# Kernel tuning notes

Hardware: AMD Instinct MI355X
Metric: run time of the kernel (lower is better)

## Reference

```python
import jax, jax.numpy as jnp
import numpy as np

MODEL_DIM = 2048
NUM_HEADS = 16
NUM_KV_HEADS = 4
HEAD_DIM = MODEL_DIM // NUM_HEADS  # 128
ROPE_BASE = 10000.0
LOCAL_WINDOW = 1024
EPS = 1.1920929e-07  # torch.finfo(float32).eps, F.rms_norm default
NEG = -1e30


def setup_inputs() -> dict:
    key = jax.random.key(0)
    ks = jax.random.split(key, 5)
    s = 0.02
    return {
        "x": jax.random.normal(ks[0], (1, 4096, MODEL_DIM), jnp.float32),
        "Wq": jax.random.normal(ks[1], (MODEL_DIM, MODEL_DIM), jnp.float32) * s,
        "Wk": jax.random.normal(ks[2], (NUM_KV_HEADS * HEAD_DIM, MODEL_DIM), jnp.float32) * s,
        "Wv": jax.random.normal(ks[3], (NUM_KV_HEADS * HEAD_DIM, MODEL_DIM), jnp.float32) * s,
        "Wo": jax.random.normal(ks[4], (MODEL_DIM, MODEL_DIM), jnp.float32) * s,
    }


def _rms_norm(x):
    return x * jax.lax.rsqrt(jnp.mean(x * x, axis=-1, keepdims=True) + EPS)


def _rope_tables(seqlen, dtype):
    inv_freq = 1.0 / (ROPE_BASE ** (jnp.arange(0, HEAD_DIM, 2, dtype=jnp.float32) / HEAD_DIM))
    freqs = jnp.arange(seqlen, dtype=jnp.float32)[:, None] * inv_freq[None, :]  # [S, hd/2]
    return jnp.cos(freqs).astype(dtype), jnp.sin(freqs).astype(dtype)


def _apply_rope(x, cos, sin):
    # x: [B, H, S, hd]; cos/sin: [S, hd/2]
    half = x.shape[-1] // 2
    x1, x2 = x[..., :half], x[..., half:]
    c = cos[None, None, :, :]
    s = sin[None, None, :, :]
    return jnp.concatenate((x1 * c + x2 * s, x2 * c - x1 * s), axis=-1)


def reference(x, Wq, Wk, Wv, Wo):
    B, S, _ = x.shape
    G = NUM_HEADS // NUM_KV_HEADS
    q = (x @ Wq.T).reshape(B, S, NUM_HEADS, HEAD_DIM).transpose(0, 2, 1, 3)
    k = (x @ Wk.T).reshape(B, S, NUM_KV_HEADS, HEAD_DIM).transpose(0, 2, 1, 3)
    v = (x @ Wv.T).reshape(B, S, NUM_KV_HEADS, HEAD_DIM).transpose(0, 2, 1, 3)
    q = _rms_norm(q)
    k = _rms_norm(k)
    cos, sin = _rope_tables(S, q.dtype)
    q = _apply_rope(q, cos, sin)
    k = _apply_rope(k, cos, sin)
    # GQA: expand kv heads to match query heads
    k = jnp.repeat(k, G, axis=1)  # [B, H, S, hd]
    v = jnp.repeat(v, G, axis=1)
    scale = 1.0 / np.sqrt(HEAD_DIM)
    scores = jnp.einsum("bhqd,bhkd->bhqk", q, k) * scale  # [B, H, S, S]
    idx = jnp.arange(S)
    causal = idx[None, :] <= idx[:, None]
    in_window = idx[None, :] > idx[:, None] - LOCAL_WINDOW
    allowed = causal & in_window  # [S, S]
    scores = jnp.where(allowed[None, None, :, :], scores, NEG)
    probs = jax.nn.softmax(scores, axis=-1)
    y = jnp.einsum("bhqk,bhkd->bhqd", probs, v)  # [B, H, S, hd]
    y = y.transpose(0, 2, 1, 3).reshape(B, S, MODEL_DIM)
    return y @ Wo.T
```

## Files before the change

kernel.cpp:

```cpp
#include <hip/hip_runtime.h>

typedef short bf16x8 __attribute__((ext_vector_type(8)));
typedef short short4v __attribute__((ext_vector_type(4)));
typedef float f32x4 __attribute__((ext_vector_type(4)));

__device__ __forceinline__ ushort f2b(float f) {
  union { float f; unsigned u; } v; v.f = f;
  unsigned r = v.u + 0x7FFF + ((v.u >> 16) & 1);
  return (ushort)(r >> 16);
}
__device__ __forceinline__ float b2f(ushort u) {
  union { unsigned u; float f; } v; v.u = ((unsigned)u) << 16;
  return v.f;
}
__device__ __forceinline__ unsigned cvtpk(float lo, float hi) {
  unsigned r;
  asm volatile("v_cvt_pk_bf16_f32 %0, %1, %2" : "=v"(r) : "v"(lo), "v"(hi));
  return r;
}
__device__ __forceinline__ f32x4 mfma16(bf16x8 a, bf16x8 b, f32x4 c) {
  return __builtin_amdgcn_mfma_f32_16x16x32_bf16(a, b, c, 0, 0, 0);
}

#define GLD_LDS16(g, l) \
  __builtin_amdgcn_global_load_lds((const __attribute__((address_space(1))) void*)(g), \
                                   (__attribute__((address_space(3))) void*)(l), 16, 0, 0)

__global__ __launch_bounds__(256) void cast_bf16(const float* __restrict__ in,
                                                 ushort* __restrict__ out, int n4) {
  int i = blockIdx.x * 256 + threadIdx.x;
  if (i >= n4) return;
  float4 f = ((const float4*)in)[i];
  ushort4 u;
  u.x = f2b(f.x); u.y = f2b(f.y); u.z = f2b(f.z); u.w = f2b(f.w);
  ((ushort4*)out)[i] = u;
}

__global__ void rope_tables_k(float* __restrict__ cosT, float* __restrict__ sinT) {
  int s = blockIdx.x, i = threadIdx.x;
  float inv = powf(10000.0f, -(float)i * (1.0f / 64.0f));
  float f = (float)s * inv;
  cosT[s * 64 + i] = cosf(f);
  sinT[s * 64 + i] = sinf(f);
}

template <bool BF16OUT>
__global__ __launch_bounds__(512) void gemm256(const ushort* __restrict__ A,
                                               const ushort* __restrict__ B,
                                               void* __restrict__ Cout,
                                               int M, int N, int K) {
  __shared__ __align__(16) ushort lds[65536];
  const int t = threadIdx.x;
  const int lane = t & 63, w = t >> 6;
  const int wr = w & 3, wc = w >> 2;
  const int l15 = lane & 15, l4 = lane >> 4;
  const int nbn = N >> 7;
  const long m0 = (long)(blockIdx.x / nbn) * 256;
  const long n0 = (long)(blockIdx.x % nbn) * 128;
  const int nk = K >> 6;

  const int rd0 = l15 * 32 + l4 * 8;
  const int rdoff = rd0 ^ ((((rd0 >> 6) & 3)) << 3);

  int arow[4], acol[4], brow[2], bcol[2];
#pragma unroll
  for (int r = 0; r < 4; ++r) {
    int us = r * 4096 + t * 8;
    int uu = us ^ (((us >> 6) & 3) << 3);
    int sub = uu >> 9;
    arow[r] = (sub >> 1) * 16 + ((uu >> 5) & 15);
    acol[r] = (sub & 1) * 32 + (uu & 31);
    if (r < 2) { brow[r] = arow[r]; bcol[r] = acol[r]; }
  }

#define STAGE_A(kk, slot)                                                      \
  do {                                                                         \
    _Pragma("unroll") for (int r = 0; r < 4; ++r)                              \
        GLD_LDS16(A + (m0 + arow[r]) * K + (kk) + acol[r],                     \
                  &lds[(slot) * 16384 + r * 4096 + t * 8]);                    \
  } while (0)
#define STAGE_B(kk, slot)                                                      \
  do {                                                                         \
    _Pragma("unroll") for (int r = 0; r < 2; ++r)                              \
        GLD_LDS16(B + (n0 + brow[r]) * K + (kk) + bcol[r],                     \
                  &lds[49152 + (slot) * 8192 + r * 4096 + t * 8]);             \
  } while (0)

  f32x4 acc[4][4] = {};

  STAGE_A(0, 0);
  STAGE_B(0, 0);
  STAGE_A(64, 1);

  for (int j = 0; j < nk; ++j) {
    const int sa = j % 3, sb = j & 1;
    asm volatile("s_waitcnt vmcnt(4)" ::: "memory");
    __builtin_amdgcn_s_barrier();

    {
      int kn = j + 1; if (kn > nk - 1) kn = nk - 1;
      STAGE_B(kn * 64, (j + 1) & 1);
    }
    bf16x8 bfrag[4][2], afrag[2][2];
#pragma unroll
    for (int n = 0; n < 4; ++n)
#pragma unroll
      for (int ks = 0; ks < 2; ++ks)
        bfrag[n][ks] = *(const bf16x8*)(&lds[49152 + sb * 8192 +
                                             ((wc * 4 + n) * 2 + ks) * 512 + rdoff]);
#pragma unroll
    for (int i = 0; i < 2; ++i)
#pragma unroll
      for (int ks = 0; ks < 2; ++ks)
        afrag[i][ks] = *(const bf16x8*)(&lds[sa * 16384 +
                                             ((wr * 4 + i) * 2 + ks) * 512 + rdoff]);
    __builtin_amdgcn_s_setprio(1);
#pragma unroll
    for (int i = 0; i < 2; ++i)
#pragma unroll
      for (int n = 0; n < 4; ++n)
#pragma unroll
        for (int ks = 0; ks < 2; ++ks)
          acc[i][n] = mfma16(afrag[i][ks], bfrag[n][ks], acc[i][n]);
    __builtin_amdgcn_s_setprio(0);
    __builtin_amdgcn_s_barrier();

    {
      int kn = j + 2; if (kn > nk - 1) kn = nk - 1;
      STAGE_A(kn * 64, (j + 2) % 3);
    }
    bf16x8 afrag1[2][2];
#pragma unroll
    for (int i = 0; i < 2; ++i)
#pragma unroll
      for (int ks = 0; ks < 2; ++ks)
        afrag1[i][ks] = *(const bf16x8*)(&lds[sa * 16384 +
                                              ((wr * 4 + i + 2) * 2 + ks) * 512 + rdoff]);
    __builtin_amdgcn_s_setprio(1);
#pragma unroll
    for (int i = 0; i < 2; ++i)
#pragma unroll
      for (int n = 0; n < 4; ++n)
#pragma unroll
        for (int ks = 0; ks < 2; ++ks)
          acc[i + 2][n] = mfma16(afrag1[i][ks], bfrag[n][ks], acc[i + 2][n]);
    __builtin_amdgcn_s_setprio(0);
  }
  asm volatile("s_waitcnt vmcnt(0)" ::: "memory");

#pragma unroll
  for (int i = 0; i < 4; ++i) {
#pragma unroll
    for (int n = 0; n < 4; ++n) {
      long mrow = m0 + wr * 64 + i * 16 + l4 * 4;
      long ncol = n0 + wc * 64 + n * 16 + l15;
#pragma unroll
      for (int r = 0; r < 4; ++r) {
        if constexpr (BF16OUT)
          ((ushort*)Cout)[(mrow + r) * N + ncol] = f2b(acc[i][n][r]);
        else
          ((float*)Cout)[(mrow + r) * N + ncol] = acc[i][n][r];
      }
    }
  }
#undef STAGE_A
#undef STAGE_B
}

__global__ __launch_bounds__(256) void postproc_k(const ushort* __restrict__ qkvb,
                                                  const float* __restrict__ cosT,
                                                  const float* __restrict__ sinT,
                                                  ushort* __restrict__ qb,
                                                  ushort* __restrict__ kb,
                                                  ushort* __restrict__ vtb) {
  const int lane = threadIdx.x & 63;
  const int s = blockIdx.x * 4 + (threadIdx.x >> 6);
  const int h = blockIdx.y;
  const int colbase = (h < 16) ? h * 128 : (h < 20 ? 2048 + (h - 16) * 128
                                                   : 2560 + (h - 20) * 128);
  const ushort* row = qkvb + (long)s * 3072 + colbase;
  float x1 = b2f(row[lane]), x2 = b2f(row[lane + 64]);
  if (h >= 20) {
    int kvh = h - 20;
    vtb[(long)(kvh * 128 + lane) * 4096 + s]      = f2b(x1);
    vtb[(long)(kvh * 128 + lane + 64) * 4096 + s] = f2b(x2);
    return;
  }
  float ss = x1 * x1 + x2 * x2;
#pragma unroll
  for (int m = 1; m < 64; m <<= 1) ss += __shfl_xor(ss, m);
  float rn = rsqrtf(ss * (1.0f / 128.0f) + 1.1920929e-07f);
  float c = cosT[s * 64 + lane], sn = sinT[s * 64 + lane];
  float x1n = x1 * rn, x2n = x2 * rn;
  float o1 = x1n * c + x2n * sn;
  float o2 = x2n * c - x1n * sn;
  if (h < 16) {
    const float scq = 0.08838834764831845f;
    ushort* dst = qb + ((long)h * 4096 + s) * 128;
    dst[lane] = f2b(o1 * scq);
    dst[lane + 64] = f2b(o2 * scq);
  } else {
    ushort* dst = kb + ((long)(h - 16) * 4096 + s) * 128;
    dst[lane] = f2b(o1);
    dst[lane + 64] = f2b(o2);
  }
}

__global__ __launch_bounds__(512) void attn_k(const ushort* __restrict__ qb,
                                              const ushort* __restrict__ kb,
                                              const ushort* __restrict__ vtb,
                                              ushort* __restrict__ yb) {
  __shared__ __align__(16) ushort lds[32768];
  const int t = threadIdx.x;
  const int lane = t & 63, w = t >> 6;
  const int l15 = lane & 15, l4 = lane >> 4;
  const int q0 = ((int)gridDim.x - 1 - (int)blockIdx.x) * 128;
  const int h = blockIdx.y, kvh = h >> 2;
  const int qw = q0 + w * 16;
  const int q = qw + l15;
  const int swz = l15 & 7;

  const ushort* Qp = qb + ((long)h * 4096 + q) * 128 + l4 * 8;
  bf16x8 qf[4];
#pragma unroll
  for (int c = 0; c < 4; ++c) qf[c] = *(const bf16x8*)(Qp + c * 32);

  const ushort* Kg = kb + (long)kvh * 4096 * 128;
  const ushort* Vg = vtb + (long)kvh * 128 * 4096;

  int kb_lo = q0 - 1023; if (kb_lo < 0) kb_lo = 0; kb_lo &= ~63;
  const int nt = (q0 + 127 - kb_lo) / 64 + 1;

  const int lbuA = (0 * 8 + w) * 512 + lane * 8;
  const int lbuB = (1 * 8 + w) * 512 + lane * 8;
  const int krA = lbuA >> 7, kcA = ((lbuA >> 3) & 15) ^ (krA & 7);
  const int krB = lbuB >> 7, kcB = ((lbuB >> 3) & 15) ^ (krB & 7);
  const int vrA = lbuA >> 6, vcA = ((lbuA >> 3) & 7) ^ (vrA & 7);
  const int vrB = lbuB >> 6, vcB = ((lbuB >> 3) & 7) ^ (vrB & 7);

#define STAGE(kbs, b)                                                        \
  do {                                                                       \
    ushort* Kl_ = &lds[(b) * 16384];                                         \
    ushort* Vl_ = &lds[(b) * 16384 + 8192];                                  \
    GLD_LDS16(Kg + (long)((kbs) + krA) * 128 + kcA * 8, Kl_ + lbuA);         \
    GLD_LDS16(Kg + (long)((kbs) + krB) * 128 + kcB * 8, Kl_ + lbuB);         \
    GLD_LDS16(Vg + (long)vrA * 4096 + (kbs) + vcA * 8, Vl_ + lbuA);          \
    GLD_LDS16(Vg + (long)vrB * 4096 + (kbs) + vcB * 8, Vl_ + lbuB);          \
  } while (0)

  f32x4 o[8] = {};
  float mrun = -1e30f, lrun = 0.0f;

  STAGE(kb_lo, 0);
  asm volatile("s_waitcnt vmcnt(0)" ::: "memory");
  __syncthreads();

  for (int ti = 0; ti < nt; ++ti) {
    const int kbs = kb_lo + ti * 64;
    const int cur = ti & 1;
    if (ti + 1 < nt) STAGE(kbs + 64, cur ^ 1);

    if (kbs + 63 >= qw - 1023 && kbs <= qw + 15) {
      const ushort* Kl = &lds[cur * 16384];
      const ushort* Vl = &lds[cur * 16384 + 8192];

      f32x4 sc[4];
#pragma unroll
      for (int st = 0; st < 4; ++st) {
        sc[st] = f32x4{0.f, 0.f, 0.f, 0.f};
        const ushort* kr = Kl + (st * 16 + l15) * 128;
#pragma unroll
        for (int c = 0; c < 4; ++c)
          sc[st] = mfma16(*(const bf16x8*)(kr + (((c * 4 + l4) ^ swz) * 8)), qf[c], sc[st]);
      }

      float s[16];
#pragma unroll
      for (int st = 0; st < 4; ++st)
#pragma unroll
        for (int r = 0; r < 4; ++r) {
          const int ki = kbs + st * 16 + l4 * 4 + r;
          s[st * 4 + r] = (ki <= q && ki > q - 1024) ? sc[st][r] : -1e30f;
        }

      float m0a = fmaxf(fmaxf(s[0], s[1]), fmaxf(s[2], s[3]));
      float m1a = fmaxf(fmaxf(s[4], s[5]), fmaxf(s[6], s[7]));
      float m2a = fmaxf(fmaxf(s[8], s[9]), fmaxf(s[10], s[11]));
      float m3a = fmaxf(fmaxf(s[12], s[13]), fmaxf(s[14], s[15]));
      float mx = fmaxf(fmaxf(m0a, m1a), fmaxf(m2a, m3a));
      mx = fmaxf(mx, __shfl_xor(mx, 16));
      mx = fmaxf(mx, __shfl_xor(mx, 32));

      float mn;
      if (__all(mx <= mrun + 8.0f)) {
        mn = mrun;
      } else {
        mn = fmaxf(mrun, mx);
        const float corr = __expf(mrun - mn);
        mrun = mn;
#pragma unroll
        for (int db = 0; db < 8; ++db)
#pragma unroll
          for (int r = 0; r < 4; ++r) o[db][r] *= corr;
        lrun *= corr;
      }

      float p[16];
#pragma unroll
      for (int j = 0; j < 16; ++j) p[j] = __expf(s[j] - mn);
      float ps = ((p[0] + p[1]) + (p[2] + p[3])) + ((p[4] + p[5]) + (p[6] + p[7]));
      ps += ((p[8] + p[9]) + (p[10] + p[11])) + ((p[12] + p[13]) + (p[14] + p[15]));
      ps += __shfl_xor(ps, 16);
      ps += __shfl_xor(ps, 32);
      lrun += ps;

      union { unsigned u[4]; bf16x8 v; } pa, pb;
      pa.u[0] = cvtpk(p[0], p[1]);   pa.u[1] = cvtpk(p[2], p[3]);
      pa.u[2] = cvtpk(p[4], p[5]);   pa.u[3] = cvtpk(p[6], p[7]);
      pb.u[0] = cvtpk(p[8], p[9]);   pb.u[1] = cvtpk(p[10], p[11]);
      pb.u[2] = cvtpk(p[12], p[13]); pb.u[3] = cvtpk(p[14], p[15]);

      const int co = 4 * (l4 & 1);
      const int c0 = (l4 >> 1) ^ swz, c1 = (2 + (l4 >> 1)) ^ swz;
      const int c2 = (4 + (l4 >> 1)) ^ swz, c3 = (6 + (l4 >> 1)) ^ swz;
#pragma unroll
      for (int db = 0; db < 8; ++db) {
        const ushort* vr = Vl + (db * 16 + l15) * 64;
        short4v a0 = *(const short4v*)(vr + c0 * 8 + co);
        short4v a1 = *(const short4v*)(vr + c1 * 8 + co);
        bf16x8 va = __builtin_shufflevector(a0, a1, 0, 1, 2, 3, 4, 5, 6, 7);
        o[db] = mfma16(va, pa.v, o[db]);
        short4v b0 = *(const short4v*)(vr + c2 * 8 + co);
        short4v b1 = *(const short4v*)(vr + c3 * 8 + co);
        bf16x8 vb = __builtin_shufflevector(b0, b1, 0, 1, 2, 3, 4, 5, 6, 7);
        o[db] = mfma16(vb, pb.v, o[db]);
      }
    }
    __syncthreads();
  }

  const float inv = 1.0f / lrun;
#pragma unroll
  for (int db = 0; db < 8; ++db)
#pragma unroll
    for (int r = 0; r < 4; ++r)
      yb[(long)q * 2048 + h * 128 + db * 16 + l4 * 4 + r] = f2b(o[db][r] * inv);
}

extern "C" void kernel_launch(void* const* d_in, const int* in_sizes, int n_in,
                              void* d_out, int out_size, void* d_ws, size_t ws_size,
                              hipStream_t stream) {
  (void)in_sizes; (void)n_in; (void)out_size; (void)ws_size;
  const float* x  = (const float*)d_in[0];
  const float* Wq = (const float*)d_in[1];
  const float* Wk = (const float*)d_in[2];
  const float* Wv = (const float*)d_in[3];
  const float* Wo = (const float*)d_in[4];
  const long S = 4096;
  ushort* ws   = (ushort*)d_ws;
  ushort* xb   = ws;
  ushort* wqkv = xb + S * 2048;
  ushort* wob  = wqkv + 3072L * 2048;
  ushort* qkvb = wob + 2048L * 2048;
  ushort* qb   = qkvb + S * 3072;
  ushort* kbuf = qb + S * 2048;
  ushort* vtb  = kbuf + 4L * 4096 * 128;
  ushort* yb   = vtb + 4L * 128 * 4096;
  float* cosT  = (float*)(yb + S * 2048);
  float* sinT  = cosT + S * 64;

  cast_bf16<<<dim3(8192), 256, 0, stream>>>(x, xb, (int)(S * 2048 / 4));
  cast_bf16<<<dim3(4096), 256, 0, stream>>>(Wq, wqkv, 2048 * 2048 / 4);
  cast_bf16<<<dim3(1024), 256, 0, stream>>>(Wk, wqkv + 2048L * 2048, 512 * 2048 / 4);
  cast_bf16<<<dim3(1024), 256, 0, stream>>>(Wv, wqkv + 2560L * 2048, 512 * 2048 / 4);
  cast_bf16<<<dim3(4096), 256, 0, stream>>>(Wo, wob, 2048 * 2048 / 4);

  gemm256<true><<<dim3(16 * 24), 512, 0, stream>>>(xb, wqkv, qkvb, 4096, 3072, 2048);
  rope_tables_k<<<dim3(4096), 64, 0, stream>>>(cosT, sinT);
  postproc_k<<<dim3(1024, 24), 256, 0, stream>>>(qkvb, cosT, sinT, qb, kbuf, vtb);
  attn_k<<<dim3(32, 16), 512, 0, stream>>>(qb, kbuf, vtb, yb);
  gemm256<false><<<dim3(16 * 16), 512, 0, stream>>>(yb, wob, d_out, 4096, 2048, 2048);
}
```

Measured before the change: 223.8 us.

## Add 256x256 QKV GEMM tile, simplify GEMM staging, skip masks on full attention tiles

Adds a 256x256-tile GEMM used for the QKV projection, launched as 192 blocks instead of 384, to raise operand reuse per block. The existing 256x128 GEMM is reworked from a triple-buffered A pipeline with XOR-swizzled LDS addressing to plain double buffering with linear LDS addressing and a single barrier pair per k-step. The attention kernel gains a fast path that skips per-element causal and window masking when a key tile lies fully inside the allowed range. Risks include more LDS bank conflicts from dropping the swizzle, fewer blocks than CUs for the QKV GEMM, and higher register pressure from the 8x4 accumulator array.

Result: slower. 248.0 us (+10.8%).

```diff
diff --git a/kernel.cpp b/kernel.cpp
--- a/kernel.cpp
+++ b/kernel.cpp
@@ -44,12 +44,108 @@
   sinT[s * 64 + i] = sinf(f);
 }
 
+
+template <bool BF16OUT>
+__global__ __launch_bounds__(512) void gemm256x256(const ushort* __restrict__ A,
+                                                   const ushort* __restrict__ B,
+                                                   void* __restrict__ Cout,
+                                                   int M, int N, int K) {
+  __shared__ __align__(16) ushort lds[65536];
+  const int t = threadIdx.x;
+  const int lane = t & 63, w = t >> 6;
+  const int wr = w & 1, wc = w >> 1;
+  const int l15 = lane & 15, l4 = lane >> 4;
+  const int nbn = N >> 8;
+  const long m0 = (long)(blockIdx.x / nbn) * 256;
+  const long n0 = (long)(blockIdx.x % nbn) * 256;
+  const int nk = K >> 6;
+
+  const int sr = ((t >> 7) << 4) + (t & 15);
+  const int sc = ((t >> 6) & 1) * 32 + ((t >> 4) & 3) * 8;
+
+#define STAGE_A2(kk, slot)                                                     \
+  do {                                                                         \
+    _Pragma("unroll") for (int r = 0; r < 4; ++r)                              \
+        GLD_LDS16(A + (m0 + r * 64 + sr) * K + (kk) + sc,                      \
+                  &lds[(slot) * 16384 + r * 4096 + t * 8]);                    \
+  } while (0)
+#define STAGE_B2(kk, slot)                                                     \
+  do {                                                                         \
+    _Pragma("unroll") for (int r = 0; r < 4; ++r)                              \
+        GLD_LDS16(B + (n0 + r * 64 + sr) * K + (kk) + sc,                      \
+                  &lds[32768 + (slot) * 16384 + r * 4096 + t * 8]);            \
+  } while (0)
+
+  f32x4 acc[8][4] = {};
+
+  STAGE_A2(0, 0);
+  STAGE_B2(0, 0);
+
+  for (int j = 0; j < nk; ++j) {
+    {
+      int kn = j + 1; if (kn > nk - 1) kn = nk - 1;
+      STAGE_A2(kn * 64, (j + 1) & 1);
+      STAGE_B2(kn * 64, (j + 1) & 1);
+    }
+    asm volatile("s_waitcnt vmcnt(8)" ::: "memory");
+    __builtin_amdgcn_s_barrier();
+    const int sa = j & 1;
+    bf16x8 bfrag[4][2];
+#pragma unroll
+    for (int n = 0; n < 4; ++n)
+#pragma unroll
+      for (int ks = 0; ks < 2; ++ks)
+        bfrag[n][ks] = *(const bf16x8*)(&lds[32768 + sa * 16384 +
+                                             ((wc * 4 + n) * 2 + ks) * 512 + lane * 8]);
+#pragma unroll
+    for (int mp = 0; mp < 4; ++mp) {
+      bf16x8 afrag[2][2];
+#pragma unroll
+      for (int i = 0; i < 2; ++i)
+#pragma unroll
+        for (int ks = 0; ks < 2; ++ks)
+          afrag[i][ks] = *(const bf16x8*)(&lds[sa * 16384 +
+                                               ((wr * 8 + mp * 2 + i) * 2 + ks) * 512 +
+                                               lane * 8]);
+      __builtin_amdgcn_s_setprio(1);
+#pragma unroll
+      for (int i = 0; i < 2; ++i)
+#pragma unroll
+        for (int n = 0; n < 4; ++n)
+#pragma unroll
+          for (int ks = 0; ks < 2; ++ks)
+            acc[mp * 2 + i][n] = mfma16(afrag[i][ks], bfrag[n][ks], acc[mp * 2 + i][n]);
+      __builtin_amdgcn_s_setprio(0);
+    }
+    __builtin_amdgcn_s_barrier();
+  }
+  asm volatile("s_waitcnt vmcnt(0)" ::: "memory");
+
+#pragma unroll
+  for (int m = 0; m < 8; ++m) {
+#pragma unroll
+    for (int n = 0; n < 4; ++n) {
+      long mrow = m0 + wr * 128 + m * 16 + l4 * 4;
+      long ncol = n0 + wc * 64 + n * 16 + l15;
+#pragma unroll
+      for (int r = 0; r < 4; ++r) {
+        if constexpr (BF16OUT)
+          ((ushort*)Cout)[(mrow + r) * N + ncol] = f2b(acc[m][n][r]);
+        else
+          ((float*)Cout)[(mrow + r) * N + ncol] = acc[m][n][r];
+      }
+    }
+  }
+#undef STAGE_A2
+#undef STAGE_B2
+}
+
 template <bool BF16OUT>
 __global__ __launch_bounds__(512) void gemm256(const ushort* __restrict__ A,
                                                const ushort* __restrict__ B,
                                                void* __restrict__ Cout,
                                                int M, int N, int K) {
-  __shared__ __align__(16) ushort lds[65536];
+  __shared__ __align__(16) ushort lds[49152];
   const int t = threadIdx.x;
   const int lane = t & 63, w = t >> 6;
   const int wr = w & 3, wc = w >> 2;
@@ -59,112 +155,84 @@
   const long n0 = (long)(blockIdx.x % nbn) * 128;
   const int nk = K >> 6;
 
-  const int rd0 = l15 * 32 + l4 * 8;
-  const int rdoff = rd0 ^ ((((rd0 >> 6) & 3)) << 3);
-
-  int arow[4], acol[4], brow[2], bcol[2];
-#pragma unroll
-  for (int r = 0; r < 4; ++r) {
-    int us = r * 4096 + t * 8;
-    int uu = us ^ (((us >> 6) & 3) << 3);
-    int sub = uu >> 9;
-    arow[r] = (sub >> 1) * 16 + ((uu >> 5) & 15);
-    acol[r] = (sub & 1) * 32 + (uu & 31);
-    if (r < 2) { brow[r] = arow[r]; bcol[r] = acol[r]; }
-  }
-
-#define STAGE_A(kk, slot)                                                      \
+  const int sr = ((t >> 7) << 4) + (t & 15);
+  const int sc = ((t >> 6) & 1) * 32 + ((t >> 4) & 3) * 8;
+
+#define STAGE_A1(kk, slot)                                                     \
   do {                                                                         \
     _Pragma("unroll") for (int r = 0; r < 4; ++r)                              \
-        GLD_LDS16(A + (m0 + arow[r]) * K + (kk) + acol[r],                     \
+        GLD_LDS16(A + (m0 + r * 64 + sr) * K + (kk) + sc,                      \
                   &lds[(slot) * 16384 + r * 4096 + t * 8]);                    \
   } while (0)
-#define STAGE_B(kk, slot)                                                      \
+#define STAGE_B1(kk, slot)                                                     \
   do {                                                                         \
     _Pragma("unroll") for (int r = 0; r < 2; ++r)                              \
-        GLD_LDS16(B + (n0 + brow[r]) * K + (kk) + bcol[r],                     \
-                  &lds[49152 + (slot) * 8192 + r * 4096 + t * 8]);             \
+        GLD_LDS16(B + (n0 + r * 64 + sr) * K + (kk) + sc,                      \
+                  &lds[32768 + (slot) * 8192 + r * 4096 + t * 8]);             \
   } while (0)
 
   f32x4 acc[4][4] = {};
 
-  STAGE_A(0, 0);
-  STAGE_B(0, 0);
-  STAGE_A(64, 1);
+  STAGE_A1(0, 0);
+  STAGE_B1(0, 0);
 
   for (int j = 0; j < nk; ++j) {
-    const int sa = j % 3, sb = j & 1;
-    asm volatile("s_waitcnt vmcnt(4)" ::: "memory");
-    __builtin_amdgcn_s_barrier();
-
     {
       int kn = j + 1; if (kn > nk - 1) kn = nk - 1;
-      STAGE_B(kn * 64, (j + 1) & 1);
-    }
-    bf16x8 bfrag[4][2], afrag[2][2];
+      STAGE_A1(kn * 64, (j + 1) & 1);
+      STAGE_B1(kn * 64, (j + 1) & 1);
+    }
+    asm volatile("s_waitcnt vmcnt(6)" ::: "memory");
+    __builtin_amdgcn_s_barrier();
+    const int sa = j & 1;
+    bf16x8 bfrag[4][2];
 #pragma unroll
     for (int n = 0; n < 4; ++n)
 #pragma unroll
       for (int ks = 0; ks < 2; ++ks)
-        bfrag[n][ks] = *(const bf16x8*)(&lds[49152 + sb * 8192 +
-                                             ((wc * 4 + n) * 2 + ks) * 512 + rdoff]);
-#pragma unroll
-    for (int i = 0; i < 2; ++i)
-#pragma unroll
-      for (int ks = 0; ks < 2; ++ks)
-        afrag[i][ks] = *(const bf16x8*)(&lds[sa * 16384 +
-                                             ((wr * 4 + i) * 2 + ks) * 512 + rdoff]);
-    __builtin_amdgcn_s_setprio(1);
-#pragma unroll
-    for (int i = 0; i < 2; ++i)
-#pragma unroll
-      for (int n = 0; n < 4; ++n)
+        bfrag[n][ks] = *(const bf16x8*)(&lds[32768 + sa * 8192 +
+                                             ((wc * 4 + n) * 2 + ks) * 512 + lane * 8]);
+#pragma unroll
+    for (int mp = 0; mp < 2; ++mp) {
+      bf16x8 afrag[2][2];
+#pragma unroll
+      for (int i = 0; i < 2; ++i)
 #pragma unroll
         for (int ks = 0; ks < 2; ++ks)
-          acc[i][n] = mfma16(afrag[i][ks], bfrag[n][ks], acc[i][n]);
-    __builtin_amdgcn_s_setprio(0);
+          afrag[i][ks] = *(const bf16x8*)(&lds[sa * 16384 +
+                                               ((wr * 4 + mp * 2 + i) * 2 + ks) * 512 +
+                                               lane * 8]);
+      __builtin_amdgcn_s_setprio(1);
+#pragma unroll
+      for (int i = 0; i < 2; ++i)
+#pragma unroll
+        for (int n = 0; n < 4; ++n)
+#pragma unroll
+          for (int ks = 0; ks < 2; ++ks)
+            acc[mp * 2 + i][n] = mfma16(afrag[i][ks], bfrag[n][ks], acc[mp * 2 + i][n]);
+      __builtin_amdgcn_s_setprio(0);
+    }
     __builtin_amdgcn_s_barrier();
-
-    {
-      int kn = j + 2; if (kn > nk - 1) kn = nk - 1;
-      STAGE_A(kn * 64, (j + 2) % 3);
-    }
-    bf16x8 afrag1[2][2];
-#pragma unroll
-    for (int i = 0; i < 2; ++i)
-#pragma unroll
-      for (int ks = 0; ks < 2; ++ks)
-        afrag1[i][ks] = *(const bf16x8*)(&lds[sa * 16384 +
-                                              ((wr * 4 + i + 2) * 2 + ks) * 512 + rdoff]);
-    __builtin_amdgcn_s_setprio(1);
-#pragma unroll
-    for (int i = 0; i < 2; ++i)
-#pragma unroll
-      for (int n = 0; n < 4; ++n)
-#pragma unroll
-        for (int ks = 0; ks < 2; ++ks)
-          acc[i + 2][n] = mfma16(afrag1[i][ks], bfrag[n][ks], acc[i + 2][n]);
-    __builtin_amdgcn_s_setprio(0);
   }
   asm volatile("s_waitcnt vmcnt(0)" ::: "memory");
 
 #pragma unroll
-  for (int i = 0; i < 4; ++i) {
+  for (int m = 0; m < 4; ++m) {
 #pragma unroll
     for (int n = 0; n < 4; ++n) {
-      long mrow = m0 + wr * 64 + i * 16 + l4 * 4;
+      long mrow = m0 + wr * 64 + m * 16 + l4 * 4;
       long ncol = n0 + wc * 64 + n * 16 + l15;
 #pragma unroll
       for (int r = 0; r < 4; ++r) {
         if constexpr (BF16OUT)
-          ((ushort*)Cout)[(mrow + r) * N + ncol] = f2b(acc[i][n][r]);
+          ((ushort*)Cout)[(mrow + r) * N + ncol] = f2b(acc[m][n][r]);
         else
-          ((float*)Cout)[(mrow + r) * N + ncol] = acc[i][n][r];
-      }
-    }
-  }
-#undef STAGE_A
-#undef STAGE_B
+          ((float*)Cout)[(mrow + r) * N + ncol] = acc[m][n][r];
+      }
+    }
+  }
+#undef STAGE_A1
+#undef STAGE_B1
 }
 
 __global__ __launch_bounds__(256) void postproc_k(const ushort* __restrict__ qkvb,
@@ -274,14 +342,22 @@
           sc[st] = mfma16(*(const bf16x8*)(kr + (((c * 4 + l4) ^ swz) * 8)), qf[c], sc[st]);
       }
 
+      const bool full = (kbs + 64 <= qw) && (kbs >= qw - 1008);
       float s[16];
-#pragma unroll
-      for (int st = 0; st < 4; ++st)
-#pragma unroll
-        for (int r = 0; r < 4; ++r) {
-          const int ki = kbs + st * 16 + l4 * 4 + r;
-          s[st * 4 + r] = (ki <= q && ki > q - 1024) ? sc[st][r] : -1e30f;
-        }
+      if (full) {
+#pragma unroll
+        for (int st = 0; st < 4; ++st)
+#pragma unroll
+          for (int r = 0; r < 4; ++r) s[st * 4 + r] = sc[st][r];
+      } else {
+#pragma unroll
+        for (int st = 0; st < 4; ++st)
+#pragma unroll
+          for (int r = 0; r < 4; ++r) {
+            const int ki = kbs + st * 16 + l4 * 4 + r;
+            s[st * 4 + r] = (ki <= q && ki > q - 1024) ? sc[st][r] : -1e30f;
+          }
+      }
 
       float m0a = fmaxf(fmaxf(s[0], s[1]), fmaxf(s[2], s[3]));
       float m1a = fmaxf(fmaxf(s[4], s[5]), fmaxf(s[6], s[7]));
@@ -375,7 +451,7 @@
   cast_bf16<<<dim3(1024), 256, 0, stream>>>(Wv, wqkv + 2560L * 2048, 512 * 2048 / 4);
   cast_bf16<<<dim3(4096), 256, 0, stream>>>(Wo, wob, 2048 * 2048 / 4);
 
-  gemm256<true><<<dim3(16 * 24), 512, 0, stream>>>(xb, wqkv, qkvb, 4096, 3072, 2048);
+  gemm256x256<true><<<dim3(16 * 12), 512, 0, stream>>>(xb, wqkv, qkvb, 4096, 3072, 2048);
   rope_tables_k<<<dim3(4096), 64, 0, stream>>>(cosT, sinT);
   postproc_k<<<dim3(1024, 24), 256, 0, stream>>>(qkvb, cosT, sinT, qb, kbuf, vtb);
   attn_k<<<dim3(32, 16), 512, 0, stream>>>(qb, kbuf, vtb, yb);
```
